# Performance work log

Hardware: AMD Instinct MI355X
Metric: run time of the kernel (lower is better)

The kernel has to match this reference:

```python
import jax, jax.numpy as jnp
import numpy as np

P = 1_048_576          # number of node pairs
MAX_STEPS = 16         # upper bound on int(euc/step)+1 for points in [0,1)^2 (sqrt(2)/0.1+1 ~ 15)
STEP = 0.1             # self.step_size
FLOW_STRENGTH = 5.0    # self.flow_strength
DEG = 3                # self.degree_polynomial


def setup_inputs() -> dict:
    key = jax.random.key(0)
    k1, k2, k3 = jax.random.split(key, 3)
    x1 = jax.random.uniform(k1, (P, 2), dtype=jnp.float32)
    x2 = jax.random.uniform(k2, (P, 2), dtype=jnp.float32)
    flow_field_parameters = jax.random.normal(k3, (DEG, 2), dtype=jnp.float32)
    return {"x1": x1, "x2": x2, "flow_field_parameters": flow_field_parameters}


def reference(x1, x2, flow_field_parameters):
    # Vectorized version of FlowEmbedder.cost over P pairs and the step loop.
    d = x2 - x1                                   # [P,2]
    euc = jnp.linalg.norm(d, axis=-1)             # [P]
    unit = d / euc[:, None]                       # [P,2] step direction * 1
    t = jnp.arange(MAX_STEPS, dtype=x1.dtype)     # [S]
    # steps_to_x2: x1 + t*0.1*(x2-x1)/euc
    pts = x1[:, None, :] + (t * STEP)[None, :, None] * unit[:, None, :]  # [P,S,2]
    x = pts[..., 0]
    y = pts[..., 1]
    # polynomial_flow_field: sum_i params[i]*comb(3,i)*x^(3-i)*y^i, i=0..2 -> comb = 1,3,3
    basis = jnp.stack([x ** 3, 3.0 * x ** 2 * y, 3.0 * x * y ** 2], axis=-1)  # [P,S,3]
    flow = jnp.einsum('psk,kc->psc', basis, flow_field_parameters)            # [P,S,2]
    dot = jnp.einsum('psc,pc->ps', flow, d)                                   # [P,S]
    e = jnp.exp(dot)
    normalizer = FLOW_STRENGTH * e / (FLOW_STRENGTH - 1.0 + e)                # [P,S]
    # mask steps t = 0 .. int(euc/step) inclusive (range(int(num_steps)+1))
    n_valid = jnp.floor(euc / STEP).astype(jnp.int32) + 1                     # [P]
    mask = jnp.arange(MAX_STEPS)[None, :] < n_valid[:, None]                  # [P,S]
    cost = jnp.sum(jnp.where(mask, STEP / normalizer, 0.0), axis=-1)          # [P]
    return cost
```

## Files before the change

kernel.cpp:

```cpp
#include <hip/hip_runtime.h>

#define NPAIRS 1048576
#define MAX_STEPS 16

__global__ __launch_bounds__(256) void flow_cost_kernel(
    const float4* __restrict__ x1,
    const float4* __restrict__ x2,
    const float*  __restrict__ params,
    float2*       __restrict__ out,
    int n2)
{
    int i = blockIdx.x * blockDim.x + threadIdx.x;
    if (i >= n2) return;

    const float p00 = params[0], p01 = params[1];
    const float p10 = params[2], p11 = params[3];
    const float p20 = params[4], p21 = params[5];

    const float4 a = x1[i];
    const float4 b = x2[i];

    float res[2];
#pragma unroll
    for (int q = 0; q < 2; ++q) {
        const float ax = q ? a.z : a.x, ay = q ? a.w : a.y;
        const float bx = q ? b.z : b.x, by = q ? b.w : b.y;
        const float dx = bx - ax, dy = by - ay;
        const float euc = sqrtf(fmaf(dx, dx, dy * dy));
        const float inv = 1.0f / euc;
        const float ux = dx * inv, uy = dy * inv;

        const float c0 =        fmaf(p00, dx, p01 * dy);
        const float c1 = 3.0f * fmaf(p10, dx, p11 * dy);
        const float c2 = 3.0f * fmaf(p20, dx, p21 * dy);

        int n_valid = (int)floorf(euc / 0.1f) + 1;
        if (n_valid > MAX_STEPS) n_valid = MAX_STEPS;

        float sum = 0.0f;
#pragma unroll
        for (int t = 0; t < MAX_STEPS; ++t) {
            const float s = 0.1f * (float)t;
            const float x = fmaf(s, ux, ax);
            const float y = fmaf(s, uy, ay);
            const float xx = x * x;
            const float xy = x * y;
            const float lin = fmaf(c0, x, c1 * y);
            const float dot = fmaf(xx, lin, c2 * xy * y);
            const float e = __expf(-dot);
            sum += (t < n_valid) ? e : 0.0f;
        }
        res[q] = fmaf(0.08f, sum, 0.02f * (float)n_valid);
    }

    out[i] = make_float2(res[0], res[1]);
}

extern "C" void kernel_launch(void* const* d_in, const int* in_sizes, int n_in,
                              void* d_out, int out_size, void* d_ws, size_t ws_size,
                              hipStream_t stream) {
    const float4* x1 = (const float4*)d_in[0];
    const float4* x2 = (const float4*)d_in[1];
    const float*  pp = (const float*)d_in[2];
    float2* out = (float2*)d_out;

    const int n2 = NPAIRS / 2;
    const int block = 256;
    const int grid = (n2 + block - 1) / block;
    flow_cost_kernel<<<grid, block, 0, stream>>>(x1, x2, pp, out, n2);
}
```

Measured before the change: 74.70 us.

## Expand flow dot product into cubic in step index and process four pairs per thread

The per-step polynomial is rewritten algebraically as a cubic in the step index t, evaluated by Horner's rule, with the -log2(e) factor folded into the coefficients so a raw exp2 intrinsic replaces expf. Each thread now handles four pairs and does a float4 store, giving more independent work per thread. The goal is fewer ALU operations per step in a compute-bound loop. The cost is higher register pressure, plus possible rounding drift from the expanded cubic compared with direct evaluation.

```diff
diff --git a/kernel.cpp b/kernel.cpp
--- a/kernel.cpp
+++ b/kernel.cpp
@@ -3,57 +3,90 @@
 #define NPAIRS 1048576
 #define MAX_STEPS 16
 
+#if __has_builtin(__builtin_amdgcn_exp2f)
+#define EXP2F(x) __builtin_amdgcn_exp2f(x)
+#else
+#define EXP2F(x) exp2f(x)
+#endif
+
 __global__ __launch_bounds__(256) void flow_cost_kernel(
     const float4* __restrict__ x1,
     const float4* __restrict__ x2,
     const float*  __restrict__ params,
-    float2*       __restrict__ out,
-    int n2)
+    float4*       __restrict__ out,
+    int n4)
 {
-    int i = blockIdx.x * blockDim.x + threadIdx.x;
-    if (i >= n2) return;
+    const int i = blockIdx.x * blockDim.x + threadIdx.x;
+    if (i >= n4) return;
 
     const float p00 = params[0], p01 = params[1];
     const float p10 = params[2], p11 = params[3];
     const float p20 = params[4], p21 = params[5];
 
-    const float4 a = x1[i];
-    const float4 b = x2[i];
+    const float4 a0 = x1[2 * i], a1 = x1[2 * i + 1];
+    const float4 b0 = x2[2 * i], b1 = x2[2 * i + 1];
 
-    float res[2];
+    const float ax[4] = {a0.x, a0.z, a1.x, a1.z};
+    const float ay[4] = {a0.y, a0.w, a1.y, a1.w};
+    const float bx[4] = {b0.x, b0.z, b1.x, b1.z};
+    const float by[4] = {b0.y, b0.w, b1.y, b1.w};
+
+    const float NL2E = -1.44269504088896340736f;
+
+    float A[4], B[4], C[4], D[4], sum[4];
+    int nv[4];
+
 #pragma unroll
-    for (int q = 0; q < 2; ++q) {
-        const float ax = q ? a.z : a.x, ay = q ? a.w : a.y;
-        const float bx = q ? b.z : b.x, by = q ? b.w : b.y;
-        const float dx = bx - ax, dy = by - ay;
-        const float euc = sqrtf(fmaf(dx, dx, dy * dy));
+    for (int q = 0; q < 4; ++q) {
+        const float dx = bx[q] - ax[q], dy = by[q] - ay[q];
+        const float s2  = fmaf(dx, dx, dy * dy);
+        const float euc = sqrtf(s2);
+        int n = (int)floorf(euc / 0.1f) + 1;
+        if (n > MAX_STEPS) n = MAX_STEPS;
+        nv[q] = n;
+
         const float inv = 1.0f / euc;
-        const float ux = dx * inv, uy = dy * inv;
+        const float u = 0.1f * dx * inv;
+        const float v = 0.1f * dy * inv;
 
-        const float c0 =        fmaf(p00, dx, p01 * dy);
-        const float c1 = 3.0f * fmaf(p10, dx, p11 * dy);
-        const float c2 = 3.0f * fmaf(p20, dx, p21 * dy);
+        const float c0 = NL2E *        fmaf(p00, dx, p01 * dy);
+        const float c1 = NL2E * 3.0f * fmaf(p10, dx, p11 * dy);
+        const float c2 = NL2E * 3.0f * fmaf(p20, dx, p21 * dy);
 
-        int n_valid = (int)floorf(euc / 0.1f) + 1;
-        if (n_valid > MAX_STEPS) n_valid = MAX_STEPS;
+        const float a = ax[q], b = ay[q];
+        const float u2 = u * u, v2 = v * v, uv = u * v;
+        const float a2 = a * a, b2 = b * b, ab = a * b;
 
-        float sum = 0.0f;
-#pragma unroll
-        for (int t = 0; t < MAX_STEPS; ++t) {
-            const float s = 0.1f * (float)t;
-            const float x = fmaf(s, ux, ax);
-            const float y = fmaf(s, uy, ay);
-            const float xx = x * x;
-            const float xy = x * y;
-            const float lin = fmaf(c0, x, c1 * y);
-            const float dot = fmaf(xx, lin, c2 * xy * y);
-            const float e = __expf(-dot);
-            sum += (t < n_valid) ? e : 0.0f;
-        }
-        res[q] = fmaf(0.08f, sum, 0.02f * (float)n_valid);
+        A[q] = fmaf(c0, u2 * u,
+               fmaf(c1, u2 * v, c2 * uv * v));
+        B[q] = fmaf(3.0f * c0, a * u2,
+               fmaf(c1, fmaf(2.0f * a, uv, b * u2),
+                    c2 * fmaf(2.0f * b, uv, a * v2)));
+        C[q] = fmaf(3.0f * c0, a2 * u,
+               fmaf(c1, fmaf(2.0f * u, ab, a2 * v),
+                    c2 * fmaf(2.0f * v, ab, b2 * u)));
+        D[q] = fmaf(c0, a2 * a,
+               fmaf(c1, a2 * b, c2 * ab * b));
+        sum[q] = 0.0f;
     }
 
-    out[i] = make_float2(res[0], res[1]);
+#pragma unroll
+    for (int t = 0; t < MAX_STEPS; ++t) {
+        const float tf = (float)t;
+#pragma unroll
+        for (int q = 0; q < 4; ++q) {
+            const float w = fmaf(fmaf(fmaf(A[q], tf, B[q]), tf, C[q]), tf, D[q]);
+            const float e = EXP2F(w);
+            sum[q] += (t < nv[q]) ? e : 0.0f;
+        }
+    }
+
+    float4 r;
+    r.x = fmaf(0.08f, sum[0], 0.02f * (float)nv[0]);
+    r.y = fmaf(0.08f, sum[1], 0.02f * (float)nv[1]);
+    r.z = fmaf(0.08f, sum[2], 0.02f * (float)nv[2]);
+    r.w = fmaf(0.08f, sum[3], 0.02f * (float)nv[3]);
+    out[i] = r;
 }
 
 extern "C" void kernel_launch(void* const* d_in, const int* in_sizes, int n_in,
@@ -62,10 +95,10 @@
     const float4* x1 = (const float4*)d_in[0];
     const float4* x2 = (const float4*)d_in[1];
     const float*  pp = (const float*)d_in[2];
-    float2* out = (float2*)d_out;
+    float4* out = (float4*)d_out;
 
-    const int n2 = NPAIRS / 2;
+    const int n4 = NPAIRS / 4;
     const int block = 256;
-    const int grid = (n2 + block - 1) / block;
-    flow_cost_kernel<<<grid, block, 0, stream>>>(x1, x2, pp, out, n2);
+    const int grid = (n4 + block - 1) / block;
+    flow_cost_kernel<<<grid, block, 0, stream>>>(x1, x2, pp, out, n4);
 }
```

New measurement: 69.30 us. 1.08x faster.
